# Optimization experiments

Hardware: AMD Instinct MI355X
Metric: run time of the kernel (lower is better)

Reference implementation:

```python
import jax, jax.numpy as jnp
import numpy as np

B, T, O, D, H = 8, 256, 16, 512, 8
HD = D // H
EPS = 1e-5


def setup_inputs() -> dict:
    key = jax.random.key(0)
    ks = jax.random.split(key, 12)
    s = 1.0 / np.sqrt(D)
    inp = {
        "organ_states": jax.random.normal(ks[0], (B, T, O, D), dtype=jnp.float32),
        "organ_mask": jax.random.randint(ks[1], (B, T, O), 0, 2) > 0,
        "Wq": jax.random.uniform(ks[2], (D, D), jnp.float32, -s, s),
        "bq": jnp.zeros((D,), jnp.float32),
        "Wk": jax.random.uniform(ks[3], (D, D), jnp.float32, -s, s),
        "bk": jnp.zeros((D,), jnp.float32),
        "Wv": jax.random.uniform(ks[4], (D, D), jnp.float32, -s, s),
        "bv": jnp.zeros((D,), jnp.float32),
        "Wo": jax.random.uniform(ks[5], (D, D), jnp.float32, -s, s),
        "bo": jnp.zeros((D,), jnp.float32),
        "gamma": jnp.ones((D,), jnp.float32),
        "beta": jnp.zeros((D,), jnp.float32),
    }
    return inp


def reference(organ_states, organ_mask, Wq, bq, Wk, bk, Wv, bv, Wo, bo, gamma, beta):
    x = organ_states  # (B, T, O, D)
    b, t, o, d = x.shape

    def heads(y):  # (B,T,O,D) -> (B,O,H,T,HD)
        return y.reshape(b, t, o, H, HD).transpose(0, 2, 3, 1, 4)

    q = heads(jnp.einsum('btod,de->btoe', x, Wq) + bq)
    k = heads(jnp.einsum('btod,de->btoe', x, Wk) + bk)
    v = heads(jnp.einsum('btod,de->btoe', x, Wv) + bv)

    scores = jnp.einsum('bohqd,bohkd->bohqk', q, k) / np.sqrt(HD).astype(np.float32)
    # key mask: (B,T,O) -> (B,O,1,1,T)
    mk = organ_mask.transpose(0, 2, 1)[:, :, None, None, :]
    scores = jnp.where(mk, scores, -jnp.inf)
    attn = jax.nn.softmax(scores, axis=-1)
    attn = jnp.where(mk, attn, 0.0)

    att = jnp.einsum('bohqk,bohkd->bohqd', attn, v)  # (B,O,H,T,HD)
    att = att.transpose(0, 3, 1, 2, 4).reshape(b, t, o, d)  # (B,T,O,D)

    out = jnp.einsum('btod,de->btoe', att, Wo) + bo
    res = out + x
    mu = jnp.mean(res, axis=-1, keepdims=True)
    var = jnp.mean(jnp.square(res - mu), axis=-1, keepdims=True)
    y = (res - mu) / jnp.sqrt(var + EPS) * gamma + beta
    y = y * organ_mask[..., None].astype(y.dtype)
    return y
```

## Files before the change

kernel.cpp:

```cpp
#include <hip/hip_runtime.h>


typedef __attribute__((ext_vector_type(8))) short bf16x8;
typedef __attribute__((ext_vector_type(4))) float f32x4;

#define MFMA16(a, b, c) __builtin_amdgcn_mfma_f32_16x16x32_bf16((a), (b), (c), 0, 0, 0)

__device__ __forceinline__ unsigned short f2bf(float f) {
  unsigned int u = __builtin_bit_cast(unsigned int, f);
  u += 0x7fffu + ((u >> 16) & 1u);
  return (unsigned short)(u >> 16);
}

__device__ __forceinline__ void gload_lds16(const void* g, void* lds) {
  __builtin_amdgcn_global_load_lds((__attribute__((address_space(1))) void*)g,
                                   (__attribute__((address_space(3))) void*)lds,
                                   16, 0, 0);
}

#define WS_XB   0ull
#define WS_WT   33554432ull
#define WS_Q    35651584ull
#define WS_K    69206016ull
#define WS_V    102760448ull
#define WS_MASK 136314880ull

__global__ void k_cvt_x(const float* __restrict__ x, unsigned short* __restrict__ xb) {
  int i = blockIdx.x * 256 + threadIdx.x;
  float4 v = ((const float4*)x)[i];
  ushort4 o;
  o.x = f2bf(v.x); o.y = f2bf(v.y); o.z = f2bf(v.z); o.w = f2bf(v.w);
  ((ushort4*)xb)[i] = o;
}

__global__ void k_prep_w(const float* __restrict__ Wq, const float* __restrict__ Wk,
                         const float* __restrict__ Wv, const float* __restrict__ Wo,
                         unsigned short* __restrict__ Wt) {
  __shared__ float tl[64][65];
  const float* src = blockIdx.z == 0 ? Wq : blockIdx.z == 1 ? Wk : blockIdx.z == 2 ? Wv : Wo;
  const int d0 = blockIdx.x * 64, e0 = blockIdx.y * 64;
  const int tid = threadIdx.x;
  {
    const int dr = tid >> 2, ec = (tid & 3) * 16;
    const float4* srow = (const float4*)(src + (size_t)(d0 + dr) * 512 + e0 + ec);
#pragma unroll
    for (int j = 0; j < 4; ++j) {
      float4 v = srow[j];
      tl[dr][ec + j * 4 + 0] = v.x;
      tl[dr][ec + j * 4 + 1] = v.y;
      tl[dr][ec + j * 4 + 2] = v.z;
      tl[dr][ec + j * 4 + 3] = v.w;
    }
  }
  __syncthreads();
  const int dd0 = (tid & 7) * 8;
#pragma unroll
  for (int i = 0; i < 2; ++i) {
    int e = i * 32 + (tid >> 3);
    bf16x8 ob;
#pragma unroll
    for (int j = 0; j < 8; ++j) ob[j] = (short)f2bf(tl[dd0 + j][e]);
    *(bf16x8*)(Wt + ((size_t)blockIdx.z * 512 + e0 + e) * 512 + d0 + dd0) = ob;
  }
}

__global__ void k_prep_mask(const void* __restrict__ mraw, unsigned char* __restrict__ mout) {
  const unsigned int* u = (const unsigned int*)mraw;
  int lane = threadIdx.x & 63;
  int packed = __any(u[lane] > 1u);
  int idx = blockIdx.x * 256 + threadIdx.x;
  unsigned char m;
  if (packed) m = ((const unsigned char*)mraw)[idx] ? 1 : 0;
  else        m = u[idx] ? 1 : 0;
  mout[idx] = m;
}

__global__ __launch_bounds__(256) void k_qkv(
    const unsigned short* __restrict__ Xb, const unsigned short* __restrict__ Wt,
    const float* __restrict__ bq, const float* __restrict__ bk, const float* __restrict__ bv,
    unsigned short* __restrict__ Qb, unsigned short* __restrict__ Kb, unsigned short* __restrict__ Vb) {
  __shared__ char sm[32768];
  const int tid = threadIdx.x, l = tid & 63, w = tid >> 6;
  const int lane15 = l & 15, quad = l >> 4;
  const int flat = blockIdx.x;
  const int mtile = flat / 12, yb = flat % 12;
  const int which = yb >> 2, ntile = yb & 3;
  const int rbase = mtile * 128;
  const char* xg = (const char*)Xb + (size_t)rbase * 1024;
  const char* wgp = (const char*)(Wt + ((size_t)which * 512 + ntile * 128) * 512);
  const int wr = w >> 1, wc = w & 1;
  const int srow = tid >> 3;
  const int c16 = (tid & 7) * 16;
  char* const abase = sm;
  char* const bbase = sm + 16384;
  f32x4 acc[4][4] = {};
  for (int ks = 0; ks < 8; ++ks) {
    __syncthreads();
#pragma unroll
    for (int i = 0; i < 4; ++i) {
      int row = i * 32 + srow;
      int swz = c16 ^ ((row & 7) << 4);
      gload_lds16(xg + (size_t)row * 1024 + ks * 128 + swz, abase + i * 4096 + w * 1024);
      gload_lds16(wgp + (size_t)row * 1024 + ks * 128 + swz, bbase + i * 4096 + w * 1024);
    }
    __syncthreads();
#pragma unroll
    for (int kc = 0; kc < 2; ++kc) {
      bf16x8 af[4], bfr[4];
#pragma unroll
      for (int mt = 0; mt < 4; ++mt) {
        int row = wr * 64 + mt * 16 + lane15;
        af[mt] = *(const bf16x8*)(abase + row * 128 + ((kc * 64 + quad * 16) ^ ((row & 7) << 4)));
      }
#pragma unroll
      for (int nt = 0; nt < 4; ++nt) {
        int col = wc * 64 + nt * 16 + lane15;
        bfr[nt] = *(const bf16x8*)(bbase + col * 128 + ((kc * 64 + quad * 16) ^ ((col & 7) << 4)));
      }
#pragma unroll
      for (int mt = 0; mt < 4; ++mt)
#pragma unroll
        for (int nt = 0; nt < 4; ++nt)
          acc[mt][nt] = MFMA16(af[mt], bfr[nt], acc[mt][nt]);
    }
  }
  const float* bias = (which == 0) ? bq : (which == 1) ? bk : bv;
  unsigned short* dst = (which == 0) ? Qb : (which == 1) ? Kb : Vb;
  const int h = ntile * 2 + wc;
#pragma unroll
  for (int mt = 0; mt < 4; ++mt) {
#pragma unroll
    for (int reg = 0; reg < 4; ++reg) {
      int r = rbase + wr * 64 + mt * 16 + quad * 4 + reg;
      int b = r >> 12, t = (r >> 4) & 255, o = r & 15;
      size_t base_bt = (size_t)((b * 16 + o) * 8 + h) * 16384 + (size_t)t * 64;
#pragma unroll
      for (int nt = 0; nt < 4; ++nt) {
        int hd = nt * 16 + lane15;
        dst[base_bt + hd] = f2bf(acc[mt][nt][reg] + bias[h * 64 + hd]);
      }
    }
  }
}

__global__ __launch_bounds__(512, 2) void k_attn(
    const unsigned short* __restrict__ Qb, const unsigned short* __restrict__ Kb,
    const unsigned short* __restrict__ Vb, const unsigned char* __restrict__ Mc,
    unsigned short* __restrict__ att) {
  __shared__ char sm[99328];
  const int tid = threadIdx.x, l = tid & 63, w = tid >> 6;
  const int lane15 = l & 15, quad = l >> 4;
  const int bid = blockIdx.x;
  const int h = bid & 7, o = (bid >> 3) & 15, b = bid >> 7;
  const size_t head = (size_t)((b * 16 + o) * 8 + h) * 16384;
  const unsigned short* qh = Qb + head;
  const char* kg = (const char*)(Kb + head);
  const unsigned short* vh = Vb + head;

  {
    const int srow = tid >> 3;
    const int c16 = (tid & 7) * 16;
    char* kdst = sm + w * 1024;
#pragma unroll
    for (int i = 0; i < 4; ++i) {
      int t = i * 64 + srow;
      gload_lds16(kg + (size_t)t * 128 + (c16 ^ ((t & 7) << 4)), kdst + i * 8192);
    }
  }
  const int q0 = w * 32;
  bf16x8 qf[2][2];
#pragma unroll
  for (int mt = 0; mt < 2; ++mt)
#pragma unroll
    for (int kc = 0; kc < 2; ++kc)
      qf[mt][kc] = *(const bf16x8*)(qh + (size_t)(q0 + mt * 16 + lane15) * 64 + kc * 32 + quad * 8);
  unsigned short vreg[32];
  {
    const int hd = tid & 63, tq = tid >> 6;
#pragma unroll
    for (int i = 0; i < 4; ++i)
#pragma unroll
      for (int j = 0; j < 8; ++j)
        vreg[i * 8 + j] = vh[(size_t)(tq * 32 + i * 8 + j) * 64 + hd];
  }
  float* maskb = (float*)(sm + 98304);
  if (tid < 256)
    maskb[tid] = Mc[(size_t)(b * 256 + tid) * 16 + o] ? 0.0f : -43280.0f;
  {
    const int hd = tid & 63, tq = tid >> 6;
    const int rowb = 32768 + hd * 512;
    const int swz = (hd & 7) << 4;
#pragma unroll
    for (int i = 0; i < 4; ++i) {
      bf16x8 pk;
#pragma unroll
      for (int j = 0; j < 8; ++j) pk[j] = (short)vreg[i * 8 + j];
      int t0 = tq * 32 + i * 8;
      *(bf16x8*)(sm + rowb + ((t0 * 2) ^ swz)) = pk;
    }
  }
  __syncthreads();

  f32x4 sacc[2][16] = {};
#pragma unroll
  for (int c = 0; c < 4; ++c) {
#pragma unroll
    for (int kc = 0; kc < 2; ++kc) {
      bf16x8 kf[4];
#pragma unroll
      for (int nt = 0; nt < 4; ++nt) {
        int t = c * 64 + nt * 16 + lane15;
        int byt = t * 128 + ((kc * 64 + quad * 16) ^ ((t & 7) << 4));
        kf[nt] = *(const bf16x8*)(sm + byt);
      }
#pragma unroll
      for (int mt = 0; mt < 2; ++mt)
#pragma unroll
        for (int nt = 0; nt < 4; ++nt)
          sacc[mt][c * 4 + nt] = MFMA16(qf[mt][kc], kf[nt], sacc[mt][c * 4 + nt]);
    }
  }

  float biasv[16];
#pragma unroll
  for (int g = 0; g < 16; ++g) biasv[g] = maskb[g * 16 + lane15];
  float inv[2][4];
#pragma unroll
  for (int mt = 0; mt < 2; ++mt) {
#pragma unroll
    for (int reg = 0; reg < 4; ++reg) {
      float v[16];
#pragma unroll
      for (int g = 0; g < 16; ++g)
        v[g] = sacc[mt][g][reg] * 0.18033688f + biasv[g];
      float m = v[0];
#pragma unroll
      for (int g = 1; g < 16; ++g) m = fmaxf(m, v[g]);
#pragma unroll
      for (int d = 1; d < 16; d <<= 1) m = fmaxf(m, __shfl_xor(m, d));
      float rs = 0.f;
#pragma unroll
      for (int g = 0; g < 16; ++g) {
        float p = __builtin_amdgcn_exp2f(v[g] - m);
        sacc[mt][g][reg] = p;
        rs += p;
      }
#pragma unroll
      for (int d = 1; d < 16; d <<= 1) rs += __shfl_xor(rs, d);
      inv[mt][reg] = 1.0f / rs;
    }
  }

  char* pb = sm + 65536 + w * 4096;
  f32x4 pv[2][4] = {};
#pragma unroll
  for (int c = 0; c < 4; ++c) {
#pragma unroll
    for (int mt = 0; mt < 2; ++mt)
#pragma unroll
      for (int nt = 0; nt < 4; ++nt)
#pragma unroll
        for (int reg = 0; reg < 4; ++reg) {
          int qrow = mt * 16 + quad * 4 + reg;
          int byt = (qrow * 128 + (nt * 16 + lane15) * 2) ^ ((qrow & 7) << 4);
          *(unsigned short*)(pb + byt) = f2bf(sacc[mt][c * 4 + nt][reg]);
        }
#pragma unroll
    for (int kc = 0; kc < 2; ++kc) {
      bf16x8 pa[2], vbr[4];
#pragma unroll
      for (int mt = 0; mt < 2; ++mt) {
        int qrow = mt * 16 + lane15;
        int byt = (qrow * 128 + kc * 64 + quad * 16) ^ ((qrow & 7) << 4);
        pa[mt] = *(const bf16x8*)(pb + byt);
      }
#pragma unroll
      for (int nh = 0; nh < 4; ++nh) {
        int hd = nh * 16 + lane15;
        int byt = hd * 512 + ((c * 128 + kc * 64 + quad * 16) ^ ((hd & 7) << 4));
        vbr[nh] = *(const bf16x8*)(sm + 32768 + byt);
      }
#pragma unroll
      for (int mt = 0; mt < 2; ++mt)
#pragma unroll
        for (int nh = 0; nh < 4; ++nh)
          pv[mt][nh] = MFMA16(pa[mt], vbr[nh], pv[mt][nh]);
    }
  }

#pragma unroll
  for (int mt = 0; mt < 2; ++mt) {
#pragma unroll
    for (int reg = 0; reg < 4; ++reg) {
      int q = q0 + mt * 16 + quad * 4 + reg;
      size_t r = (size_t)(b * 256 + q) * 16 + o;
      float iv = inv[mt][reg];
#pragma unroll
      for (int nh = 0; nh < 4; ++nh)
        att[r * 512 + h * 64 + nh * 16 + lane15] = f2bf(pv[mt][nh][reg] * iv);
    }
  }
}

__global__ __launch_bounds__(512) void k_oproj(
    const unsigned short* __restrict__ A, const unsigned short* __restrict__ Wt,
    const float* __restrict__ bo, const float* __restrict__ X,
    const unsigned char* __restrict__ Mc, const float* __restrict__ gamma,
    const float* __restrict__ beta, float* __restrict__ out) {
  __shared__ char sm[73728];
  __shared__ float psum[64][8];
  __shared__ float psumsq[64][8];
  __shared__ float smean[64];
  __shared__ float srstd[64];
  const int tid = threadIdx.x, l = tid & 63, w = tid >> 6;
  const int lane15 = l & 15, quad = l >> 4;
  const int rbase = blockIdx.x * 64;
  const char* ag = (const char*)A;
  const char* wgp = (const char*)(Wt + (size_t)1536 * 512);
  const int srow = tid >> 3;
  const int c16 = (tid & 7) * 16;
  const int swz_a = c16 ^ ((srow & 7) << 4);
  char* adst = sm + w * 1024;
  f32x4 acc[4][4] = {};
  for (int ks = 0; ks < 8; ++ks) {
    __syncthreads();
    gload_lds16(ag + (size_t)(rbase + srow) * 1024 + ks * 128 + swz_a, adst);
#pragma unroll
    for (int p = 0; p < 8; ++p) {
      int er = p * 64 + srow;
      gload_lds16(wgp + (size_t)er * 1024 + ks * 128 + (c16 ^ ((er & 7) << 4)),
                  sm + 8192 + p * 8192 + w * 1024);
    }
    __syncthreads();
#pragma unroll
    for (int kc = 0; kc < 2; ++kc) {
      bf16x8 af[4], bfr[4];
#pragma unroll
      for (int mt = 0; mt < 4; ++mt) {
        int row = mt * 16 + lane15;
        int byt = (row * 128 + kc * 64 + quad * 16) ^ ((row & 7) << 4);
        af[mt] = *(const bf16x8*)(sm + byt);
      }
#pragma unroll
      for (int nt = 0; nt < 4; ++nt) {
        int col = w * 64 + nt * 16 + lane15;
        int byt = (col * 128 + kc * 64 + quad * 16) ^ ((col & 7) << 4);
        bfr[nt] = *(const bf16x8*)(sm + 8192 + byt);
      }
#pragma unroll
      for (int mt = 0; mt < 4; ++mt)
#pragma unroll
        for (int nt = 0; nt < 4; ++nt)
          acc[mt][nt] = MFMA16(af[mt], bfr[nt], acc[mt][nt]);
    }
  }
#pragma unroll
  for (int mt = 0; mt < 4; ++mt) {
#pragma unroll
    for (int reg = 0; reg < 4; ++reg) {
      int rl = mt * 16 + quad * 4 + reg;
      int r = rbase + rl;
      float s1 = 0.f, s2 = 0.f;
#pragma unroll
      for (int nt = 0; nt < 4; ++nt) {
        int col = w * 64 + nt * 16 + lane15;
        float v = acc[mt][nt][reg] + bo[col] + X[(size_t)r * 512 + col];
        acc[mt][nt][reg] = v;
        s1 += v; s2 += v * v;
      }
#pragma unroll
      for (int d = 1; d < 16; d <<= 1) { s1 += __shfl_xor(s1, d); s2 += __shfl_xor(s2, d); }
      if (lane15 == 0) { psum[rl][w] = s1; psumsq[rl][w] = s2; }
    }
  }
  __syncthreads();
  if (tid < 64) {
    float a = 0.f, q = 0.f;
#pragma unroll
    for (int j = 0; j < 8; ++j) { a += psum[tid][j]; q += psumsq[tid][j]; }
    float mu = a * (1.f / 512.f);
    float var = q * (1.f / 512.f) - mu * mu;
    smean[tid] = mu;
    srstd[tid] = rsqrtf(fmaxf(var, 0.f) + 1e-5f);
  }
  __syncthreads();
#pragma unroll
  for (int mt = 0; mt < 4; ++mt) {
#pragma unroll
    for (int reg = 0; reg < 4; ++reg) {
      int rl = mt * 16 + quad * 4 + reg;
      int r = rbase + rl;
      float mu = smean[rl], rs = srstd[rl];
      float mkf = Mc[r] ? 1.f : 0.f;
#pragma unroll
      for (int nt = 0; nt < 4; ++nt) {
        int col = w * 64 + nt * 16 + lane15;
        float y = (acc[mt][nt][reg] - mu) * rs * gamma[col] + beta[col];
        out[(size_t)r * 512 + col] = y * mkf;
      }
    }
  }
}

extern "C" void kernel_launch(void* const* d_in, const int* in_sizes, int n_in,
                              void* d_out, int out_size, void* d_ws, size_t ws_size,
                              hipStream_t stream) {
  const float* X     = (const float*)d_in[0];
  const void*  Mraw  = d_in[1];
  const float* Wq    = (const float*)d_in[2];
  const float* bq    = (const float*)d_in[3];
  const float* Wk    = (const float*)d_in[4];
  const float* bk    = (const float*)d_in[5];
  const float* Wv    = (const float*)d_in[6];
  const float* bv    = (const float*)d_in[7];
  const float* Wo    = (const float*)d_in[8];
  const float* bo    = (const float*)d_in[9];
  const float* gamma = (const float*)d_in[10];
  const float* beta  = (const float*)d_in[11];

  char* ws = (char*)d_ws;
  unsigned short* Xb  = (unsigned short*)(ws + WS_XB);
  unsigned short* Wt  = (unsigned short*)(ws + WS_WT);
  unsigned short* Qb  = (unsigned short*)(ws + WS_Q);
  unsigned short* Kb  = (unsigned short*)(ws + WS_K);
  unsigned short* Vb  = (unsigned short*)(ws + WS_V);
  unsigned char*  Mc  = (unsigned char*)(ws + WS_MASK);
  unsigned short* att = Xb;

  hipLaunchKernelGGL(k_cvt_x,    dim3(16384),   dim3(256), 0, stream, X, Xb);
  hipLaunchKernelGGL(k_prep_w,   dim3(8, 8, 4), dim3(256), 0, stream, Wq, Wk, Wv, Wo, Wt);
  hipLaunchKernelGGL(k_prep_mask,dim3(128),     dim3(256), 0, stream, Mraw, Mc);
  hipLaunchKernelGGL(k_qkv,      dim3(3072),    dim3(256), 0, stream, Xb, Wt, bq, bk, bv, Qb, Kb, Vb);
  hipLaunchKernelGGL(k_attn,     dim3(1024),    dim3(512), 0, stream, Qb, Kb, Vb, Mc, att);
  hipLaunchKernelGGL(k_oproj,    dim3(512),     dim3(512), 0, stream, att, Wt, bo, X, Mc, gamma, beta,
                     (float*)d_out);
}
```

Measured before the change: 297.5 us.

## Double-buffer LDS staging in QKV and O-proj GEMMs; retile QKV to full-width rows

The QKV projection changes from 128x128 tiles with 256 threads to 64-row by 512-column tiles with 512 threads, one wave per head, matching the O-projection layout. Both GEMMs now use double-buffered LDS (144 KB) so the next K-slice is loaded while MFMAs run on the current one, with one barrier per iteration instead of two. The attention kernel reuses the K region of LDS for the P buffer after an added barrier, cutting its LDS from about 97 KB to 65 KB. The aim is to hide global-load latency and let more attention blocks fit per CU, at the cost of one QKV/O-proj block per CU because of the larger LDS use.

Result: slower. 314.2 us (+5.6%).

```diff
diff --git a/kernel.cpp b/kernel.cpp
--- a/kernel.cpp
+++ b/kernel.cpp
@@ -75,47 +75,48 @@
   mout[idx] = m;
 }
 
-__global__ __launch_bounds__(256) void k_qkv(
+__global__ __launch_bounds__(512) void k_qkv(
     const unsigned short* __restrict__ Xb, const unsigned short* __restrict__ Wt,
     const float* __restrict__ bq, const float* __restrict__ bk, const float* __restrict__ bv,
     unsigned short* __restrict__ Qb, unsigned short* __restrict__ Kb, unsigned short* __restrict__ Vb) {
-  __shared__ char sm[32768];
+  __shared__ char sm[147456];
   const int tid = threadIdx.x, l = tid & 63, w = tid >> 6;
   const int lane15 = l & 15, quad = l >> 4;
-  const int flat = blockIdx.x;
-  const int mtile = flat / 12, yb = flat % 12;
-  const int which = yb >> 2, ntile = yb & 3;
-  const int rbase = mtile * 128;
-  const char* xg = (const char*)Xb + (size_t)rbase * 1024;
-  const char* wgp = (const char*)(Wt + ((size_t)which * 512 + ntile * 128) * 512);
-  const int wr = w >> 1, wc = w & 1;
+  const int rbase = blockIdx.x * 64, which = blockIdx.y;
+  const char* xg = (const char*)Xb;
+  const char* wgp = (const char*)(Wt + (size_t)which * 512 * 512);
   const int srow = tid >> 3;
   const int c16 = (tid & 7) * 16;
-  char* const abase = sm;
-  char* const bbase = sm + 16384;
+  const int swz_a = c16 ^ ((srow & 7) << 4);
+
+  auto STAGE = [&](int ks, char* buf) {
+    gload_lds16(xg + (size_t)(rbase + srow) * 1024 + ks * 128 + swz_a, buf + w * 1024);
+#pragma unroll
+    for (int p = 0; p < 8; ++p) {
+      int er = p * 64 + srow;
+      gload_lds16(wgp + (size_t)er * 1024 + ks * 128 + (c16 ^ ((er & 7) << 4)),
+                  buf + 8192 + p * 8192 + w * 1024);
+    }
+  };
+
+  STAGE(0, sm);
+  __syncthreads();
   f32x4 acc[4][4] = {};
   for (int ks = 0; ks < 8; ++ks) {
-    __syncthreads();
-#pragma unroll
-    for (int i = 0; i < 4; ++i) {
-      int row = i * 32 + srow;
-      int swz = c16 ^ ((row & 7) << 4);
-      gload_lds16(xg + (size_t)row * 1024 + ks * 128 + swz, abase + i * 4096 + w * 1024);
-      gload_lds16(wgp + (size_t)row * 1024 + ks * 128 + swz, bbase + i * 4096 + w * 1024);
-    }
-    __syncthreads();
+    char* cur = sm + (ks & 1) * 73728;
+    if (ks < 7) STAGE(ks + 1, sm + ((ks + 1) & 1) * 73728);
 #pragma unroll
     for (int kc = 0; kc < 2; ++kc) {
       bf16x8 af[4], bfr[4];
 #pragma unroll
       for (int mt = 0; mt < 4; ++mt) {
-        int row = wr * 64 + mt * 16 + lane15;
-        af[mt] = *(const bf16x8*)(abase + row * 128 + ((kc * 64 + quad * 16) ^ ((row & 7) << 4)));
-      }
-#pragma unroll
-      for (int nt = 0; nt < 4; ++nt) {
-        int col = wc * 64 + nt * 16 + lane15;
-        bfr[nt] = *(const bf16x8*)(bbase + col * 128 + ((kc * 64 + quad * 16) ^ ((col & 7) << 4)));
+        int row = mt * 16 + lane15;
+        af[mt] = *(const bf16x8*)(cur + row * 128 + ((kc * 64 + quad * 16) ^ ((row & 7) << 4)));
+      }
+#pragma unroll
+      for (int nt = 0; nt < 4; ++nt) {
+        int col = w * 64 + nt * 16 + lane15;
+        bfr[nt] = *(const bf16x8*)(cur + 8192 + col * 128 + ((kc * 64 + quad * 16) ^ ((col & 7) << 4)));
       }
 #pragma unroll
       for (int mt = 0; mt < 4; ++mt)
@@ -123,21 +124,22 @@
         for (int nt = 0; nt < 4; ++nt)
           acc[mt][nt] = MFMA16(af[mt], bfr[nt], acc[mt][nt]);
     }
+    __syncthreads();
   }
   const float* bias = (which == 0) ? bq : (which == 1) ? bk : bv;
   unsigned short* dst = (which == 0) ? Qb : (which == 1) ? Kb : Vb;
-  const int h = ntile * 2 + wc;
 #pragma unroll
   for (int mt = 0; mt < 4; ++mt) {
 #pragma unroll
     for (int reg = 0; reg < 4; ++reg) {
-      int r = rbase + wr * 64 + mt * 16 + quad * 4 + reg;
+      int r = rbase + mt * 16 + quad * 4 + reg;
       int b = r >> 12, t = (r >> 4) & 255, o = r & 15;
-      size_t base_bt = (size_t)((b * 16 + o) * 8 + h) * 16384 + (size_t)t * 64;
-#pragma unroll
-      for (int nt = 0; nt < 4; ++nt) {
-        int hd = nt * 16 + lane15;
-        dst[base_bt + hd] = f2bf(acc[mt][nt][reg] + bias[h * 64 + hd]);
+      size_t base_bt = (size_t)((b * 16 + o) * 8 + w) * 16384 + (size_t)t * 64;
+#pragma unroll
+      for (int nt = 0; nt < 4; ++nt) {
+        int e = w * 64 + nt * 16 + lane15;
+        float v = acc[mt][nt][reg] + bias[e];
+        dst[base_bt + nt * 16 + lane15] = f2bf(v);
       }
     }
   }
@@ -147,7 +149,7 @@
     const unsigned short* __restrict__ Qb, const unsigned short* __restrict__ Kb,
     const unsigned short* __restrict__ Vb, const unsigned char* __restrict__ Mc,
     unsigned short* __restrict__ att) {
-  __shared__ char sm[99328];
+  __shared__ char sm[66560];
   const int tid = threadIdx.x, l = tid & 63, w = tid >> 6;
   const int lane15 = l & 15, quad = l >> 4;
   const int bid = blockIdx.x;
@@ -183,7 +185,7 @@
       for (int j = 0; j < 8; ++j)
         vreg[i * 8 + j] = vh[(size_t)(tq * 32 + i * 8 + j) * 64 + hd];
   }
-  float* maskb = (float*)(sm + 98304);
+  float* maskb = (float*)(sm + 65536);
   if (tid < 256)
     maskb[tid] = Mc[(size_t)(b * 256 + tid) * 16 + o] ? 0.0f : -43280.0f;
   {
@@ -220,6 +222,7 @@
           sacc[mt][c * 4 + nt] = MFMA16(qf[mt][kc], kf[nt], sacc[mt][c * 4 + nt]);
     }
   }
+  __syncthreads();
 
   float biasv[16];
 #pragma unroll
@@ -251,7 +254,7 @@
     }
   }
 
-  char* pb = sm + 65536 + w * 4096;
+  char* pb = sm + w * 4096;
   f32x4 pv[2][4] = {};
 #pragma unroll
   for (int c = 0; c < 4; ++c) {
@@ -307,7 +310,7 @@
     const float* __restrict__ bo, const float* __restrict__ X,
     const unsigned char* __restrict__ Mc, const float* __restrict__ gamma,
     const float* __restrict__ beta, float* __restrict__ out) {
-  __shared__ char sm[73728];
+  __shared__ char sm[147456];
   __shared__ float psum[64][8];
   __shared__ float psumsq[64][8];
   __shared__ float smean[64];
@@ -320,32 +323,35 @@
   const int srow = tid >> 3;
   const int c16 = (tid & 7) * 16;
   const int swz_a = c16 ^ ((srow & 7) << 4);
-  char* adst = sm + w * 1024;
-  f32x4 acc[4][4] = {};
-  for (int ks = 0; ks < 8; ++ks) {
-    __syncthreads();
-    gload_lds16(ag + (size_t)(rbase + srow) * 1024 + ks * 128 + swz_a, adst);
+
+  auto STAGE = [&](int ks, char* buf) {
+    gload_lds16(ag + (size_t)(rbase + srow) * 1024 + ks * 128 + swz_a, buf + w * 1024);
 #pragma unroll
     for (int p = 0; p < 8; ++p) {
       int er = p * 64 + srow;
       gload_lds16(wgp + (size_t)er * 1024 + ks * 128 + (c16 ^ ((er & 7) << 4)),
-                  sm + 8192 + p * 8192 + w * 1024);
-    }
-    __syncthreads();
+                  buf + 8192 + p * 8192 + w * 1024);
+    }
+  };
+
+  STAGE(0, sm);
+  __syncthreads();
+  f32x4 acc[4][4] = {};
+  for (int ks = 0; ks < 8; ++ks) {
+    char* cur = sm + (ks & 1) * 73728;
+    if (ks < 7) STAGE(ks + 1, sm + ((ks + 1) & 1) * 73728);
 #pragma unroll
     for (int kc = 0; kc < 2; ++kc) {
       bf16x8 af[4], bfr[4];
 #pragma unroll
       for (int mt = 0; mt < 4; ++mt) {
         int row = mt * 16 + lane15;
-        int byt = (row * 128 + kc * 64 + quad * 16) ^ ((row & 7) << 4);
-        af[mt] = *(const bf16x8*)(sm + byt);
+        af[mt] = *(const bf16x8*)(cur + row * 128 + ((kc * 64 + quad * 16) ^ ((row & 7) << 4)));
       }
 #pragma unroll
       for (int nt = 0; nt < 4; ++nt) {
         int col = w * 64 + nt * 16 + lane15;
-        int byt = (col * 128 + kc * 64 + quad * 16) ^ ((col & 7) << 4);
-        bfr[nt] = *(const bf16x8*)(sm + 8192 + byt);
+        bfr[nt] = *(const bf16x8*)(cur + 8192 + col * 128 + ((kc * 64 + quad * 16) ^ ((col & 7) << 4)));
       }
 #pragma unroll
       for (int mt = 0; mt < 4; ++mt)
@@ -353,6 +359,7 @@
         for (int nt = 0; nt < 4; ++nt)
           acc[mt][nt] = MFMA16(af[mt], bfr[nt], acc[mt][nt]);
     }
+    __syncthreads();
   }
 #pragma unroll
   for (int mt = 0; mt < 4; ++mt) {
@@ -430,7 +437,7 @@
   hipLaunchKernelGGL(k_cvt_x,    dim3(16384),   dim3(256), 0, stream, X, Xb);
   hipLaunchKernelGGL(k_prep_w,   dim3(8, 8, 4), dim3(256), 0, stream, Wq, Wk, Wv, Wo, Wt);
   hipLaunchKernelGGL(k_prep_mask,dim3(128),     dim3(256), 0, stream, Mraw, Mc);
-  hipLaunchKernelGGL(k_qkv,      dim3(3072),    dim3(256), 0, stream, Xb, Wt, bq, bk, bv, Qb, Kb, Vb);
+  hipLaunchKernelGGL(k_qkv,      dim3(512, 3),  dim3(512), 0, stream, Xb, Wt, bq, bk, bv, Qb, Kb, Vb);
   hipLaunchKernelGGL(k_attn,     dim3(1024),    dim3(512), 0, stream, Qb, Kb, Vb, Mc, att);
   hipLaunchKernelGGL(k_oproj,    dim3(512),     dim3(512), 0, stream, att, Wt, bo, X, Mc, gamma, beta,
                      (float*)d_out);
```
